# Optimization experiments

Hardware: AMD Instinct MI355X
Metric: run time of the kernel (lower is better)

Reference implementation:

```python
import jax, jax.numpy as jnp
import numpy as np

STRIDE, PAD, DIL, KH, KW = 1, 1, 1, 3, 3


def _bilinear_gather(img, y, xq):
    # img: (Cin,H,W); y,xq: (K,Ho,Wo) float sample coords. Zero padding outside.
    H, W = img.shape[1], img.shape[2]
    y0 = jnp.floor(y); x0 = jnp.floor(xq)
    wy1 = y - y0; wx1 = xq - x0
    wy0 = 1.0 - wy1; wx0 = 1.0 - wx1

    def g(yi, xi):
        valid = (yi >= 0) & (yi <= H - 1) & (xi >= 0) & (xi <= W - 1)
        yc = jnp.clip(yi, 0, H - 1).astype(jnp.int32)
        xc = jnp.clip(xi, 0, W - 1).astype(jnp.int32)
        v = img[:, yc, xc]  # (Cin,K,Ho,Wo)
        return jnp.where(valid[None], v, 0.0)

    return ((wy0 * wx0)[None] * g(y0, x0) + (wy0 * wx1)[None] * g(y0, x0 + 1)
            + (wy1 * wx0)[None] * g(y0 + 1, x0) + (wy1 * wx1)[None] * g(y0 + 1, x0 + 1))


def _deform_conv2d(x, offset, weight, bias):
    B, Cin, H, W = x.shape
    Cout = weight.shape[0]
    Ho, Wo = offset.shape[2], offset.shape[3]
    K = KH * KW
    off = offset.reshape(B, K, 2, Ho, Wo)  # (y,x) pairs per kernel tap, row-major
    ki, kj = jnp.meshgrid(jnp.arange(KH), jnp.arange(KW), indexing='ij')
    base_y = (jnp.arange(Ho) * STRIDE - PAD)[None, :, None] + (ki.reshape(K) * DIL)[:, None, None]  # (K,Ho,1)
    base_x = (jnp.arange(Wo) * STRIDE - PAD)[None, None, :] + (kj.reshape(K) * DIL)[:, None, None]  # (K,1,Wo)
    ys = base_y.astype(x.dtype) + off[:, :, 0]  # (B,K,Ho,Wo)
    xs = base_x.astype(x.dtype) + off[:, :, 1]
    samples = jax.vmap(_bilinear_gather)(x, ys, xs)  # (B,Cin,K,Ho,Wo)
    out = jnp.einsum('bckhw,ock->bohw', samples, weight.reshape(Cout, Cin, K))
    return out + bias[None, :, None, None]


def setup_inputs() -> dict:
    key = jax.random.key(0)
    k1, k2, k3, k4, k5 = jax.random.split(key, 5)
    x = jax.random.normal(k1, (8, 64, 96, 96), dtype=jnp.float32)
    offset = jax.random.normal(k2, (8, 18, 96, 96), dtype=jnp.float32)
    x2 = jax.random.normal(k3, (8, 64, 96, 96), dtype=jnp.float32)
    weight = jax.random.normal(k4, (64, 64, 3, 3), dtype=jnp.float32) * 0.04  # ~kaiming scale for fan_in=576
    bias = jax.random.normal(k5, (64,), dtype=jnp.float32) * 0.1
    return {'x': x, 'offset': offset, 'x2': x2, 'weight': weight, 'bias': bias}


def reference(x, offset, x2, weight, bias):
    out = _deform_conv2d(x, offset, weight, bias)
    out = out + x2
    return jnp.clip(out, 0.0, 6.0)  # ReLU6
```

## Files before the change

### kernel.cpp

```cpp
#include <hip/hip_runtime.h>
#include <math.h>

#define B_    8
#define CIN   64
#define COUT  64
#define H_    96
#define W_    96
#define HW    9216
#define KK    9
#define PIX   64
#define NTHR  256
#define BLKS_PER_B 144
#define SP    72

typedef __attribute__((ext_vector_type(8))) short short8;
typedef __attribute__((ext_vector_type(4))) float floatx4;

#if __has_builtin(__builtin_amdgcn_fdot2_f32_bf16)
#define HAVE_DOT2 1
typedef __attribute__((ext_vector_type(2))) __bf16 bf16x2;
static __device__ __forceinline__ bf16x2 as_bf16x2(unsigned u) {
    union { unsigned u; bf16x2 v; } c; c.u = u; return c.v;
}
#else
#define HAVE_DOT2 0
#endif

static __device__ __forceinline__ unsigned short f2bf(float f) {
    unsigned u = __float_as_uint(f);
    unsigned r = (u + 0x7FFFu + ((u >> 16) & 1u)) >> 16;
    return (unsigned short)r;
}
static __device__ __forceinline__ float bf_lo(unsigned u) { return __uint_as_float(u << 16); }
static __device__ __forceinline__ float bf_hi(unsigned u) { return __uint_as_float(u & 0xFFFF0000u); }

static __device__ __forceinline__ unsigned pack_bf2(float vl, float vh) {
    unsigned rl = __float_as_uint(vl) + 0x8000u;
    unsigned rh = __float_as_uint(vh) + 0x8000u;
    return __builtin_amdgcn_perm(rh, rl, 0x07060302u);
}

__global__ __launch_bounds__(256) void prep_kernel(const float* __restrict__ x,
                                                   const float* __restrict__ w,
                                                   unsigned int* __restrict__ xTu,
                                                   unsigned short* __restrict__ wA) {
    __shared__ float tile[64][65];
    if (blockIdx.x < B_ * BLKS_PER_B) {
        int b   = blockIdx.x / BLKS_PER_B;
        int hw0 = (blockIdx.x % BLKS_PER_B) * 64;
        int lane = threadIdx.x & 63;
        int r    = threadIdx.x >> 6;
        const float* xb = x + (size_t)b * CIN * HW;
        #pragma unroll
        for (int i = 0; i < 16; ++i) {
            int c = r + i * 4;
            tile[c][lane] = xb[(size_t)c * HW + hw0 + lane];
        }
        __syncthreads();
        unsigned int* dst = xTu + ((size_t)b * HW + hw0) * 32;
        int c2 = threadIdx.x & 31;
        int pr = threadIdx.x >> 5;
        #pragma unroll
        for (int i = 0; i < 8; ++i) {
            int p = pr + i * 8;
            unsigned pk = (unsigned)f2bf(tile[2 * c2][p]) |
                          ((unsigned)f2bf(tile[2 * c2 + 1][p]) << 16);
            dst[(size_t)p * 32 + c2] = pk;
        }
    } else {
        int gid  = (blockIdx.x - B_ * BLKS_PER_B) * 256 + threadIdx.x;
        int lane = gid & 63;
        int wq   = (gid >> 6) & 3;
        int kap  = gid >> 8;
        int o    = wq * 16 + (lane & 15);
        int cb   = (kap & 1) * 32 + (lane >> 4) * 8;
        int tap  = kap >> 1;
        short8 v;
        #pragma unroll
        for (int j = 0; j < 8; ++j)
            v[j] = (short)f2bf(w[o * 576 + (cb + j) * 9 + tap]);
        *(short8*)&wA[(size_t)gid * 8] = v;
    }
}

static __device__ __forceinline__ void issue_tap_loads(
    const unsigned int* __restrict__ xb, const ushort4* eoS,
    int t, int wq, int half, int c2, unsigned u[8][4])
{
    #pragma unroll
    for (int j = 0; j < 8; ++j) {
        int p = wq * 16 + j * 2 + half;
        ushort4 o4 = eoS[t * 64 + p];
        u[j][0] = xb[((size_t)o4.x << 5) + c2];
        u[j][1] = xb[((size_t)o4.y << 5) + c2];
        u[j][2] = xb[((size_t)o4.z << 5) + c2];
        u[j][3] = xb[((size_t)o4.w << 5) + c2];
    }
}

#if HAVE_DOT2
static __device__ __forceinline__ void compute_tap(
    const uint2* awP, short* Sbuf, int t, int wq, int half, int c2,
    const unsigned u[8][4])
{
    unsigned int* Su = (unsigned int*)Sbuf;
    #pragma unroll
    for (int j = 0; j < 8; ++j) {
        int p = wq * 16 + j * 2 + half;
        uint2 aw = awP[t * 64 + p];
        unsigned lo01 = __builtin_amdgcn_perm(u[j][1], u[j][0], 0x05040100u);
        unsigned hi01 = __builtin_amdgcn_perm(u[j][1], u[j][0], 0x07060302u);
        unsigned lo23 = __builtin_amdgcn_perm(u[j][3], u[j][2], 0x05040100u);
        unsigned hi23 = __builtin_amdgcn_perm(u[j][3], u[j][2], 0x07060302u);
        float vl = __builtin_amdgcn_fdot2_f32_bf16(as_bf16x2(lo01), as_bf16x2(aw.x), 0.0f, false);
        vl = __builtin_amdgcn_fdot2_f32_bf16(as_bf16x2(lo23), as_bf16x2(aw.y), vl, false);
        float vh = __builtin_amdgcn_fdot2_f32_bf16(as_bf16x2(hi01), as_bf16x2(aw.x), 0.0f, false);
        vh = __builtin_amdgcn_fdot2_f32_bf16(as_bf16x2(hi23), as_bf16x2(aw.y), vh, false);
        Su[p * (SP / 2) + c2] = pack_bf2(vl, vh);
    }
}
#else
static __device__ __forceinline__ void compute_tap(
    const float4* ewP, short* Sbuf, int t, int wq, int half, int c2,
    const unsigned u[8][4])
{
    unsigned int* Su = (unsigned int*)Sbuf;
    #pragma unroll
    for (int j = 0; j < 8; ++j) {
        int p = wq * 16 + j * 2 + half;
        float4 w4 = ewP[t * 64 + p];
        float vl = w4.x * bf_lo(u[j][0]);
        vl = fmaf(w4.y, bf_lo(u[j][1]), vl);
        vl = fmaf(w4.z, bf_lo(u[j][2]), vl);
        vl = fmaf(w4.w, bf_lo(u[j][3]), vl);
        float vh = w4.x * bf_hi(u[j][0]);
        vh = fmaf(w4.y, bf_hi(u[j][1]), vh);
        vh = fmaf(w4.z, bf_hi(u[j][2]), vh);
        vh = fmaf(w4.w, bf_hi(u[j][3]), vh);
        Su[p * (SP / 2) + c2] = pack_bf2(vl, vh);
    }
}
#endif

__global__ __launch_bounds__(256, 4) void deform_mfma_kernel(
    const unsigned int* __restrict__ xTu, const float* __restrict__ offset,
    const float* __restrict__ x2, const float* __restrict__ bias,
    const unsigned short* __restrict__ wA, float* __restrict__ out)
{
#if HAVE_DOT2
    __shared__ uint2   awP[KK * PIX];
#else
    __shared__ float4  awP[KK * PIX];
#endif
    __shared__ ushort4 eoS[KK * PIX];
    __shared__ __align__(16) short S[2][PIX * SP];

    const int tid  = threadIdx.x;
    const int b    = blockIdx.x & 7;
    const int pix0 = (blockIdx.x >> 3) * PIX;
    const int lane = tid & 63;
    const int wq   = __builtin_amdgcn_readfirstlane(tid >> 6);

    const unsigned int* xb = xTu + (size_t)b * HW * 32;
    const float* offb = offset + (size_t)b * (18 * HW);

    const short8* wAv = (const short8*)wA;
    const int abase = wq * 64 + lane;

    short8 a0 = wAv[abase];
    short8 a1 = wAv[abase + 4 * 64];

    for (int e = tid; e < KK * PIX; e += NTHR) {
        int k  = e >> 6;
        int p  = e & 63;
        int hw = pix0 + p;
        int h  = hw / W_;
        int w  = hw - h * W_;
        float offy = offb[(size_t)(2 * k) * HW + hw];
        float offx = offb[(size_t)(2 * k + 1) * HW + hw];
        int ki = k / 3;
        int kj = k - ki * 3;
        float yy = (float)(h - 1 + ki) + offy;
        float xx = (float)(w - 1 + kj) + offx;
        float y0f = floorf(yy), x0f = floorf(xx);
        float wy1 = yy - y0f, wx1 = xx - x0f;
        float wy0 = 1.0f - wy1, wx0 = 1.0f - wx1;
        int y0 = (int)y0f, x0 = (int)x0f;
        int y1 = y0 + 1, x1 = x0 + 1;
        float ay0 = (y0 >= 0 && y0 < H_) ? wy0 : 0.0f;
        float ay1 = (y1 >= 0 && y1 < H_) ? wy1 : 0.0f;
        float ax0 = (x0 >= 0 && x0 < W_) ? wx0 : 0.0f;
        float ax1 = (x1 >= 0 && x1 < W_) ? wx1 : 0.0f;
        float w00 = ay0 * ax0, w01 = ay0 * ax1, w10 = ay1 * ax0, w11 = ay1 * ax1;
        int y0c = min(max(y0, 0), H_ - 1), y1c = min(max(y1, 0), H_ - 1);
        int x0c = min(max(x0, 0), W_ - 1), x1c = min(max(x1, 0), W_ - 1);
#if HAVE_DOT2
        awP[e] = make_uint2((unsigned)f2bf(w00) | ((unsigned)f2bf(w01) << 16),
                            (unsigned)f2bf(w10) | ((unsigned)f2bf(w11) << 16));
#else
        awP[e] = make_float4(w00, w01, w10, w11);
#endif
        eoS[e] = make_ushort4((unsigned short)(y0c * W_ + x0c),
                              (unsigned short)(y0c * W_ + x1c),
                              (unsigned short)(y1c * W_ + x0c),
                              (unsigned short)(y1c * W_ + x1c));
    }

    floatx4 acc[4];
    #pragma unroll
    for (int nt = 0; nt < 4; ++nt) acc[nt] = (floatx4){0.f, 0.f, 0.f, 0.f};

    __syncthreads();

    const int c2   = lane & 31;
    const int half = lane >> 5;

    unsigned u[8][4];
    issue_tap_loads(xb, eoS, 0, wq, half, c2, u);

    for (int t = 0; t < KK; ++t) {
        const int buf = t & 1;

        compute_tap(awP, &S[buf][0], t, wq, half, c2, u);
        __syncthreads();

        short8 n0, n1;
        if (t < KK - 1) {
            issue_tap_loads(xb, eoS, t + 1, wq, half, c2, u);
            n0 = wAv[abase + (8 * (t + 1)) * 64];
            n1 = wAv[abase + (8 * (t + 1) + 4) * 64];
        }

        {
            const int n = lane & 15;
            const int qk = (lane >> 4) * 8;
            #pragma unroll
            for (int nt = 0; nt < 4; ++nt) {
                int p = nt * 16 + n;
                short8 b0 = *(const short8*)&S[buf][p * SP + qk];
                short8 b1 = *(const short8*)&S[buf][p * SP + 32 + qk];
                acc[nt] = __builtin_amdgcn_mfma_f32_16x16x32_bf16(a0, b0, acc[nt], 0, 0, 0);
                acc[nt] = __builtin_amdgcn_mfma_f32_16x16x32_bf16(a1, b1, acc[nt], 0, 0, 0);
            }
        }

        a0 = n0;
        a1 = n1;
    }

    {
        const int n = lane & 15;
        const int orow = wq * 16 + (lane >> 4) * 4;
        float bia[4];
        #pragma unroll
        for (int reg = 0; reg < 4; ++reg) bia[reg] = bias[orow + reg];
        #pragma unroll
        for (int nt = 0; nt < 4; ++nt) {
            int hw = pix0 + nt * 16 + n;
            #pragma unroll
            for (int reg = 0; reg < 4; ++reg) {
                size_t idx = ((size_t)(b * COUT + orow + reg)) * HW + hw;
                float r = acc[nt][reg] + bia[reg] + x2[idx];
                r = fminf(fmaxf(r, 0.0f), 6.0f);
                out[idx] = r;
            }
        }
    }
}

__global__ __launch_bounds__(256, 4) void deform_nchw_kernel(
    const float* __restrict__ x, const float* __restrict__ offset,
    const float* __restrict__ x2, const float* __restrict__ weight,
    const float* __restrict__ bias, float* __restrict__ out)
{
    __shared__ float sT[CIN * PIX];
    __shared__ float ewS[4][KK * PIX];
    __shared__ int   eoS[4][KK * PIX];

    const int tid  = threadIdx.x;
    const int b    = blockIdx.x / BLKS_PER_B;
    const int pix0 = (blockIdx.x % BLKS_PER_B) * PIX;
    const int lane = tid & 63;
    const int wq   = __builtin_amdgcn_readfirstlane(tid >> 6);

    const float* xb   = x + (size_t)b * (CIN * HW);
    const float* offb = offset + (size_t)b * (18 * HW);

    for (int e = tid; e < KK * PIX; e += NTHR) {
        int k  = e >> 6;
        int p  = e & 63;
        int hw = pix0 + p;
        int h  = hw / W_;
        int w  = hw - h * W_;
        float offy = offb[(size_t)(2 * k) * HW + hw];
        float offx = offb[(size_t)(2 * k + 1) * HW + hw];
        int ki = k / 3;
        int kj = k - ki * 3;
        float yy = (float)(h - 1 + ki) + offy;
        float xx = (float)(w - 1 + kj) + offx;
        float y0f = floorf(yy), x0f = floorf(xx);
        float wy1 = yy - y0f, wx1 = xx - x0f;
        float wy0 = 1.0f - wy1, wx0 = 1.0f - wx1;
        int y0 = (int)y0f, x0 = (int)x0f;
        int y1 = y0 + 1, x1 = x0 + 1;
        float vy0 = (y0 >= 0 && y0 < H_) ? 1.0f : 0.0f;
        float vy1 = (y1 >= 0 && y1 < H_) ? 1.0f : 0.0f;
        float vx0 = (x0 >= 0 && x0 < W_) ? 1.0f : 0.0f;
        float vx1 = (x1 >= 0 && x1 < W_) ? 1.0f : 0.0f;
        int y0c = min(max(y0, 0), H_ - 1), y1c = min(max(y1, 0), H_ - 1);
        int x0c = min(max(x0, 0), W_ - 1), x1c = min(max(x1, 0), W_ - 1);
        ewS[0][e] = wy0 * wx0 * vy0 * vx0;
        ewS[1][e] = wy0 * wx1 * vy0 * vx1;
        ewS[2][e] = wy1 * wx0 * vy1 * vx0;
        ewS[3][e] = wy1 * wx1 * vy1 * vx1;
        eoS[0][e] = y0c * W_ + x0c;
        eoS[1][e] = y0c * W_ + x1c;
        eoS[2][e] = y1c * W_ + x0c;
        eoS[3][e] = y1c * W_ + x1c;
    }

    float acc[16];
    #pragma unroll
    for (int i = 0; i < 16; ++i) acc[i] = 0.0f;

    __syncthreads();

    for (int k = 0; k < KK; ++k) {
        {
            const int eb = k * 64 + lane;
            const float w0 = ewS[0][eb], w1 = ewS[1][eb], w2 = ewS[2][eb], w3 = ewS[3][eb];
            const int   o0 = eoS[0][eb], o1 = eoS[1][eb], o2 = eoS[2][eb], o3 = eoS[3][eb];
            const int cg = tid >> 6;
            const float* xc = xb + (size_t)(cg * 16) * HW;
            #pragma unroll
            for (int i = 0; i < 16; ++i) {
                float v = w0 * xc[o0] + w1 * xc[o1] + w2 * xc[o2] + w3 * xc[o3];
                sT[(cg * 16 + i) * 64 + lane] = v;
                xc += HW;
            }
        }
        __syncthreads();
        {
            #pragma unroll 2
            for (int c = 0; c < 64; ++c) {
                float sv = sT[c * 64 + lane];
                #pragma unroll
                for (int oi = 0; oi < 16; ++oi)
                    acc[oi] = fmaf(weight[(wq * 16 + oi) * 576 + c * 9 + k], sv, acc[oi]);
            }
        }
        __syncthreads();
    }

    const size_t obase = ((size_t)b * COUT + wq * 16) * HW + pix0 + lane;
    #pragma unroll
    for (int oi = 0; oi < 16; ++oi) {
        float r = acc[oi] + bias[wq * 16 + oi] + x2[obase + (size_t)oi * HW];
        r = fminf(fmaxf(r, 0.0f), 6.0f);
        out[obase + (size_t)oi * HW] = r;
    }
}

extern "C" void kernel_launch(void* const* d_in, const int* in_sizes, int n_in,
                              void* d_out, int out_size, void* d_ws, size_t ws_size,
                              hipStream_t stream) {
    const float* x      = (const float*)d_in[0];
    const float* offset = (const float*)d_in[1];
    const float* x2     = (const float*)d_in[2];
    const float* weight = (const float*)d_in[3];
    const float* bias   = (const float*)d_in[4];
    float* out          = (float*)d_out;

    const int grid = B_ * BLKS_PER_B;

    const size_t xT_bytes = (size_t)B_ * HW * CIN * sizeof(unsigned short);
    const size_t wA_bytes = (size_t)18 * 4 * 64 * 8 * sizeof(unsigned short);

    if (ws_size >= xT_bytes + wA_bytes) {
        unsigned int*   xTu = (unsigned int*)d_ws;
        unsigned short* wA  = (unsigned short*)((char*)d_ws + xT_bytes);
        prep_kernel<<<grid + 18, 256, 0, stream>>>(x, weight, xTu, wA);
        deform_mfma_kernel<<<grid, NTHR, 0, stream>>>(xTu, offset, x2, bias, wA, out);
    } else {
        deform_nchw_kernel<<<grid, NTHR, 0, stream>>>(x, offset, x2, weight, bias, out);
    }
}
```

Measured before the change: 118.0 us.

## Double-buffer tap gather registers and prefetch residual before final MFMA

The gathered tap values now sit in two register buffers, so the loads for tap t+1 are issued before the bilinear combine of tap t rather than after the barrier. This lets global gather latency overlap the combine, the shared-memory store and the MFMA work. The x2 residual is also loaded early, during the last tap iteration, so it is not fetched only in the epilogue. Occupancy hint drops from 4 to 3 blocks per CU to leave room for the doubled registers, which may cut latency hiding across waves.

```diff
diff --git a/kernel.cpp b/kernel.cpp
--- a/kernel.cpp
+++ b/kernel.cpp
@@ -85,7 +85,7 @@
 
 static __device__ __forceinline__ void issue_tap_loads(
     const unsigned int* __restrict__ xb, const ushort4* eoS,
-    int t, int wq, int half, int c2, unsigned u[8][4])
+    int t, int wq, int half, int c2, unsigned (&u)[8][4])
 {
     #pragma unroll
     for (int j = 0; j < 8; ++j) {
@@ -101,7 +101,7 @@
 #if HAVE_DOT2
 static __device__ __forceinline__ void compute_tap(
     const uint2* awP, short* Sbuf, int t, int wq, int half, int c2,
-    const unsigned u[8][4])
+    const unsigned (&u)[8][4])
 {
     unsigned int* Su = (unsigned int*)Sbuf;
     #pragma unroll
@@ -122,7 +122,7 @@
 #else
 static __device__ __forceinline__ void compute_tap(
     const float4* ewP, short* Sbuf, int t, int wq, int half, int c2,
-    const unsigned u[8][4])
+    const unsigned (&u)[8][4])
 {
     unsigned int* Su = (unsigned int*)Sbuf;
     #pragma unroll
@@ -142,7 +142,7 @@
 }
 #endif
 
-__global__ __launch_bounds__(256, 4) void deform_mfma_kernel(
+__global__ __launch_bounds__(256, 3) void deform_mfma_kernel(
     const unsigned int* __restrict__ xTu, const float* __restrict__ offset,
     const float* __restrict__ x2, const float* __restrict__ bias,
     const unsigned short* __restrict__ wA, float* __restrict__ out)
@@ -215,28 +215,40 @@
     const int c2   = lane & 31;
     const int half = lane >> 5;
 
-    unsigned u[8][4];
-    issue_tap_loads(xb, eoS, 0, wq, half, c2, u);
+    unsigned u[2][8][4];
+    issue_tap_loads(xb, eoS, 0, wq, half, c2, u[0]);
+
+    float x2r[4][4];
+    const int n_     = lane & 15;
+    const int orow   = wq * 16 + (lane >> 4) * 4;
+    const size_t ob0 = ((size_t)(b * COUT + orow)) * HW + pix0 + n_;
 
     for (int t = 0; t < KK; ++t) {
         const int buf = t & 1;
 
-        compute_tap(awP, &S[buf][0], t, wq, half, c2, u);
-        __syncthreads();
-
         short8 n0, n1;
         if (t < KK - 1) {
-            issue_tap_loads(xb, eoS, t + 1, wq, half, c2, u);
+            issue_tap_loads(xb, eoS, t + 1, wq, half, c2, u[(t + 1) & 1]);
             n0 = wAv[abase + (8 * (t + 1)) * 64];
             n1 = wAv[abase + (8 * (t + 1) + 4) * 64];
         }
 
+        compute_tap(awP, &S[buf][0], t, wq, half, c2, u[buf]);
+        __syncthreads();
+
+        if (t == KK - 1) {
+            #pragma unroll
+            for (int nt = 0; nt < 4; ++nt)
+                #pragma unroll
+                for (int reg = 0; reg < 4; ++reg)
+                    x2r[nt][reg] = x2[ob0 + (size_t)reg * HW + nt * 16];
+        }
+
         {
-            const int n = lane & 15;
             const int qk = (lane >> 4) * 8;
             #pragma unroll
             for (int nt = 0; nt < 4; ++nt) {
-                int p = nt * 16 + n;
+                int p = nt * 16 + n_;
                 short8 b0 = *(const short8*)&S[buf][p * SP + qk];
                 short8 b1 = *(const short8*)&S[buf][p * SP + 32 + qk];
                 acc[nt] = __builtin_amdgcn_mfma_f32_16x16x32_bf16(a0, b0, acc[nt], 0, 0, 0);
@@ -249,18 +261,15 @@
     }
 
     {
-        const int n = lane & 15;
-        const int orow = wq * 16 + (lane >> 4) * 4;
         float bia[4];
         #pragma unroll
         for (int reg = 0; reg < 4; ++reg) bia[reg] = bias[orow + reg];
         #pragma unroll
         for (int nt = 0; nt < 4; ++nt) {
-            int hw = pix0 + nt * 16 + n;
             #pragma unroll
             for (int reg = 0; reg < 4; ++reg) {
-                size_t idx = ((size_t)(b * COUT + orow + reg)) * HW + hw;
-                float r = acc[nt][reg] + bia[reg] + x2[idx];
+                size_t idx = ob0 + (size_t)reg * HW + nt * 16;
+                float r = acc[nt][reg] + bia[reg] + x2r[nt][reg];
                 r = fminf(fmaxf(r, 0.0f), 6.0f);
                 out[idx] = r;
             }
```

Result: slower. 218.5 us (+85.2%).
